# Performance work log

Hardware: AMD Instinct MI355X
Metric: run time of the kernel (lower is better)

Reference implementation:

```python
import jax, jax.numpy as jnp
import numpy as np

D = 1024   # n_embd
H = 16     # n_head
HD = D // H

def setup_inputs() -> dict:
    key = jax.random.key(0)
    ks = jax.random.split(key, 6)
    s = 1.0 / np.sqrt(D)
    x  = jax.random.normal(ks[0], (4, 2048, D), dtype=jnp.float32)
    Wq = jax.random.uniform(ks[1], (D, D), jnp.float32, -s, s)
    Wk = jax.random.uniform(ks[2], (D, D), jnp.float32, -s, s)
    Wv = jax.random.uniform(ks[3], (D, D), jnp.float32, -s, s)
    Wp = jax.random.uniform(ks[4], (D, D), jnp.float32, -s, s)
    bp = jax.random.uniform(ks[5], (D,),   jnp.float32, -s, s)
    return {"x": x, "Wq": Wq, "Wk": Wk, "Wv": Wv, "Wp": Wp, "bp": bp}

def reference(x, Wq, Wk, Wv, Wp, bp):
    B, T, C = x.shape
    scale = 1.0 / np.sqrt(HD)
    # torch nn.Linear: y = x @ W.T
    q = (x @ Wq.T).reshape(B, T, H, HD).transpose(0, 2, 1, 3)  # [B,H,T,hd]
    k = (x @ Wk.T).reshape(B, T, H, HD).transpose(0, 2, 1, 3)
    v = (x @ Wv.T).reshape(B, T, H, HD).transpose(0, 2, 1, 3)
    att = jnp.einsum('bhqd,bhkd->bhqk', q, k) * scale           # [B,H,T,T]
    causal = jnp.tril(jnp.ones((T, T), dtype=bool))
    att = jnp.where(causal[None, None], att, -jnp.inf)
    att = jax.nn.softmax(att, axis=-1)
    y = jnp.einsum('bhqk,bhkd->bhqd', att, v)                   # [B,H,T,hd]
    y = y.transpose(0, 2, 1, 3).reshape(B, T, C)
    return y @ Wp.T + bp
```

## Files before the change

kernel.cpp:

```cpp
#include <hip/hip_runtime.h>
#include <hip/hip_bf16.h>
#include <math.h>


#define B_  4
#define T_  2048
#define D_  1024
#define H_  16
#define HD_ 64
#define M_  (B_ * T_)

typedef short bf16x8 __attribute__((ext_vector_type(8)));
typedef float f32x4  __attribute__((ext_vector_type(4)));

__device__ __forceinline__ f32x4 mfma16(bf16x8 a, bf16x8 b, f32x4 c) {
    return __builtin_amdgcn_mfma_f32_16x16x32_bf16(a, b, c, 0, 0, 0);
}

__device__ __forceinline__ void gl_lds16(const unsigned short* g, unsigned short* l) {
    __builtin_amdgcn_global_load_lds(
        (const __attribute__((address_space(1))) void*)g,
        (__attribute__((address_space(3))) void*)l, 16, 0, 0);
}

__device__ __forceinline__ unsigned short f2bf(float f) {
    union { __hip_bfloat16 h; unsigned short u; } cv;
    cv.h = __float2bfloat16(f);
    return cv.u;
}
__device__ __forceinline__ float bf2f(unsigned short u) {
    return __uint_as_float(((unsigned)u) << 16);
}
__device__ __forceinline__ float exp2_fast(float x) {
    return __builtin_amdgcn_exp2f(x);
}

struct su4 { unsigned short x, y, z, w; };

__global__ __launch_bounds__(256)
void cvt_all_kernel(const float* __restrict__ x,
                    const float* __restrict__ Wq, const float* __restrict__ Wk,
                    const float* __restrict__ Wv, const float* __restrict__ Wp,
                    unsigned short* __restrict__ dst) {
    const int i = blockIdx.x * 256 + threadIdx.x;
    const float* src;
    int j;
    if (i < 2097152) {
        src = x; j = i;
    } else {
        const int k = i - 2097152;
        const int wsel = k >> 18;
        j = k & 262143;
        src = (wsel == 0) ? Wq : (wsel == 1) ? Wk : (wsel == 2) ? Wv : Wp;
    }
    const float4 v = ((const float4*)src)[j];
    su4 o;
    o.x = f2bf(v.x); o.y = f2bf(v.y); o.z = f2bf(v.z); o.w = f2bf(v.w);
    ((su4*)dst)[i] = o;
}

__global__ __launch_bounds__(256, 2)
void qkv_kernel(const unsigned short* __restrict__ X,
                const unsigned short* __restrict__ Wq,
                const unsigned short* __restrict__ Wk,
                const unsigned short* __restrict__ Wv,
                unsigned short* __restrict__ Qo,
                unsigned short* __restrict__ Ko,
                unsigned short* __restrict__ Vo)
{
    __shared__ unsigned short As[128 * 64];
    __shared__ unsigned short Bs[128 * 64];

    const int m0 = blockIdx.x * 128;
    const int by = blockIdx.y;
    const unsigned short* W = (by < 8) ? Wq : (by < 16) ? Wk : Wv;
    unsigned short*       O = (by < 8) ? Qo : (by < 16) ? Ko : Vo;
    const int n0   = (by & 7) * 128;
    const bool vsec = (by >= 16);
    const int tid  = threadIdx.x;
    const int lane = tid & 63;
    const int wv   = tid >> 6;
    const int wr   = (wv >> 1) * 64;
    const int wc   = (wv & 1) * 64;
    const int g    = lane >> 4;
    const int c    = lane & 15;

    f32x4 acc[4][4] = {};

    for (int k0 = 0; k0 < D_; k0 += 64) {
        #pragma unroll
        for (int i = 0; i < 4; ++i) {
            const int flat = i * 2048 + tid * 8;
            const int row = flat >> 6, col = flat & 63;
            gl_lds16(X + (size_t)(m0 + row) * D_ + k0 + col, As + flat);
            gl_lds16(W + (size_t)(n0 + row) * D_ + k0 + col, Bs + flat);
        }
        __syncthreads();
        #pragma unroll
        for (int kk = 0; kk < 64; kk += 32) {
            bf16x8 af[4], bg[4];
            #pragma unroll
            for (int mi = 0; mi < 4; ++mi)
                af[mi] = *(const bf16x8*)(As + (wr + mi * 16 + c) * 64 + kk + g * 8);
            #pragma unroll
            for (int ni = 0; ni < 4; ++ni)
                bg[ni] = *(const bf16x8*)(Bs + (wc + ni * 16 + c) * 64 + kk + g * 8);
            if (!vsec) {
                #pragma unroll
                for (int mi = 0; mi < 4; ++mi)
                    #pragma unroll
                    for (int ni = 0; ni < 4; ++ni)
                        acc[mi][ni] = mfma16(af[mi], bg[ni], acc[mi][ni]);
            } else {
                #pragma unroll
                for (int mi = 0; mi < 4; ++mi)
                    #pragma unroll
                    for (int ni = 0; ni < 4; ++ni)
                        acc[mi][ni] = mfma16(bg[ni], af[mi], acc[mi][ni]);
            }
        }
        __syncthreads();
    }

    if (!vsec) {
        #pragma unroll
        for (int mi = 0; mi < 4; ++mi)
            #pragma unroll
            for (int ni = 0; ni < 4; ++ni)
                #pragma unroll
                for (int r = 0; r < 4; ++r) {
                    const int m = m0 + wr + mi * 16 + g * 4 + r;
                    const int n = n0 + wc + ni * 16 + c;
                    const int b = m >> 11, t = m & (T_ - 1);
                    const int h = n >> 6,  hd = n & 63;
                    O[((size_t)((b << 4) + h) * T_ + t) * HD_ + hd] = f2bf(acc[mi][ni][r]);
                }
    } else {
        #pragma unroll
        for (int mi = 0; mi < 4; ++mi)
            #pragma unroll
            for (int ni = 0; ni < 4; ++ni)
                #pragma unroll
                for (int r = 0; r < 4; ++r) {
                    const int n = n0 + wc + ni * 16 + g * 4 + r;
                    const int m = m0 + wr + mi * 16 + c;
                    const int b = m >> 11, t = m & (T_ - 1);
                    const int h = n >> 6,  hd = n & 63;
                    O[((size_t)((b << 4) + h) * HD_ + hd) * T_ + t] = f2bf(acc[mi][ni][r]);
                }
    }
}

__device__ __forceinline__ bf16x8 ptrans(const f32x4& p0, const f32x4& p1,
                                         int lane, int g, int c) {
    unsigned int P32[2][2];
    P32[0][0] = (unsigned int)f2bf(p0[0]) | ((unsigned int)f2bf(p0[1]) << 16);
    P32[0][1] = (unsigned int)f2bf(p0[2]) | ((unsigned int)f2bf(p0[3]) << 16);
    P32[1][0] = (unsigned int)f2bf(p1[0]) | ((unsigned int)f2bf(p1[1]) << 16);
    P32[1][1] = (unsigned int)f2bf(p1[2]) | ((unsigned int)f2bf(p1[3]) << 16);
    const int sl0 = c + ((lane & 16) << 1);
    const int sl1 = sl0 + 16;
    const int q00 = __shfl((int)P32[0][0], sl0), q10 = __shfl((int)P32[1][0], sl0);
    const int q01 = __shfl((int)P32[0][1], sl0), q11 = __shfl((int)P32[1][1], sl0);
    const int q02 = __shfl((int)P32[0][0], sl1), q12 = __shfl((int)P32[1][0], sl1);
    const int q03 = __shfl((int)P32[0][1], sl1), q13 = __shfl((int)P32[1][1], sl1);
    const bool nhi = (g & 2) != 0;
    union { unsigned int u[4]; bf16x8 v; } pf;
    pf.u[0] = nhi ? q10 : q00;
    pf.u[1] = nhi ? q11 : q01;
    pf.u[2] = nhi ? q12 : q02;
    pf.u[3] = nhi ? q13 : q03;
    return pf.v;
}

__global__ __launch_bounds__(256, 4)
void attn_kernel(const unsigned short* __restrict__ Q,
                 const unsigned short* __restrict__ K,
                 const unsigned short* __restrict__ VT,
                 unsigned short* __restrict__ Y)
{
    __shared__ unsigned short Ks[2][4096];
    __shared__ unsigned short Vs[2][4096];

    const int bh = blockIdx.x;
    const int qt = 31 - blockIdx.y;
    const unsigned short* Qp  = Q  + (size_t)bh * T_ * HD_;
    const unsigned short* Kp  = K  + (size_t)bh * T_ * HD_;
    const unsigned short* VTp = VT + (size_t)bh * HD_ * T_;
    const int b = bh >> 4, h = bh & 15;

    const int tid  = threadIdx.x;
    const int lane = tid & 63;
    const int w    = tid >> 6;
    const int g    = lane >> 4;
    const int c    = lane & 15;
    const float SC = 0.18033688011112042f;

    const int qw = qt * 64 + w * 16;
    const int nt = qt + 1;

    int srow[2], scol[2];
    #pragma unroll
    for (int i = 0; i < 2; ++i) {
        const int L = (i * 256 + tid) * 16;
        srow[i] = L >> 7;
        scol[i] = (L & 127) ^ ((srow[i] & 7) << 4);
    }

    bf16x8 qf[2];
    #pragma unroll
    for (int dk = 0; dk < 2; ++dk) {
        bf16x8 t = *(const bf16x8*)(Qp + (size_t)(qw + c) * HD_ + dk * 32 + g * 8);
        #pragma unroll
        for (int j = 0; j < 8; ++j)
            t[j] = (short)f2bf(bf2f((unsigned short)t[j]) * SC);
        qf[dk] = t;
    }

    float m_l = -1e30f, l_l = 0.f;
    f32x4 oacc[4] = {};
    const int swz = (c & 7) << 4;

    auto stage = [&](int buf, int tb) {
        #pragma unroll
        for (int i = 0; i < 2; ++i) {
            const int L = (i * 256 + tid) * 16;
            gl_lds16(Kp + (size_t)(tb + srow[i]) * HD_ + (scol[i] >> 1),
                     &Ks[buf][L >> 1]);
            gl_lds16(VTp + (size_t)srow[i] * T_ + tb + (scol[i] >> 1),
                     &Vs[buf][L >> 1]);
        }
    };

    auto compute = [&](const unsigned short* Kbuf, const unsigned short* Vbuf,
                       int tb, bool last) {
        const char* Kb = (const char*)Kbuf;
        const char* Vb = (const char*)Vbuf;

        __builtin_amdgcn_s_setprio(1);

        f32x4 sA[2] = {}, sB[2] = {};
        #pragma unroll
        for (int ni = 0; ni < 2; ++ni)
            #pragma unroll
            for (int dk = 0; dk < 2; ++dk) {
                const int col = (dk * 64 + g * 16) ^ swz;
                const bf16x8 kA = *(const bf16x8*)(Kb + (ni * 16 + c) * 128 + col);
                const bf16x8 kB = *(const bf16x8*)(Kb + (32 + ni * 16 + c) * 128 + col);
                sA[ni] = mfma16(kA, qf[dk], sA[ni]);
                sB[ni] = mfma16(kB, qf[dk], sB[ni]);
            }

        if (last) {
            #pragma unroll
            for (int ni = 0; ni < 2; ++ni)
                #pragma unroll
                for (int r = 0; r < 4; ++r) {
                    const int kA = tb + ni * 16 + g * 4 + r;
                    sA[ni][r] = (kA      <= qw + c) ? sA[ni][r] : -1e30f;
                    sB[ni][r] = (kA + 32 <= qw + c) ? sB[ni][r] : -1e30f;
                }
        }

        float pmax = sA[0][0];
        #pragma unroll
        for (int ni = 0; ni < 2; ++ni)
            #pragma unroll
            for (int r = 0; r < 4; ++r) {
                pmax = fmaxf(pmax, sA[ni][r]);
                pmax = fmaxf(pmax, sB[ni][r]);
            }
        pmax = fmaxf(pmax, __shfl_xor(pmax, 16));
        pmax = fmaxf(pmax, __shfl_xor(pmax, 32));

        const bool skip = __all(pmax - m_l <= 8.0f);
        float al = 1.f;
        if (!skip) {
            const float mn = fmaxf(m_l, pmax);
            al = exp2_fast(m_l - mn);
            m_l = mn;
        }

        float rs = 0.f;
        #pragma unroll
        for (int ni = 0; ni < 2; ++ni)
            #pragma unroll
            for (int r = 0; r < 4; ++r) {
                const float eA = exp2_fast(sA[ni][r] - m_l);
                const float eB = exp2_fast(sB[ni][r] - m_l);
                sA[ni][r] = eA; sB[ni][r] = eB;
                rs += eA + eB;
            }
        rs += __shfl_xor(rs, 16);
        rs += __shfl_xor(rs, 32);
        l_l = l_l * al + rs;

        const bf16x8 pfA = ptrans(sA[0], sA[1], lane, g, c);
        const bf16x8 pfB = ptrans(sB[0], sB[1], lane, g, c);

        #pragma unroll
        for (int dn = 0; dn < 4; ++dn) {
            const int row = dn * 16 + c;
            const bf16x8 vA = *(const bf16x8*)(Vb + row * 128 + ((g * 16)      ^ swz));
            const bf16x8 vB = *(const bf16x8*)(Vb + row * 128 + ((64 + g * 16) ^ swz));
            if (!skip) {
                #pragma unroll
                for (int r = 0; r < 4; ++r)
                    oacc[dn][r] *= al;
            }
            oacc[dn] = mfma16(vA, pfA, oacc[dn]);
            oacc[dn] = mfma16(vB, pfB, oacc[dn]);
        }

        __builtin_amdgcn_s_setprio(0);
    };

    stage(0, 0);
    __syncthreads();
    int ti = 0;
    for (;;) {
        if (ti + 1 < nt) stage(1, (ti + 1) << 6);
        compute(Ks[0], Vs[0], ti << 6, ti == nt - 1);
        __syncthreads();
        if (++ti >= nt) break;

        if (ti + 1 < nt) stage(0, (ti + 1) << 6);
        compute(Ks[1], Vs[1], ti << 6, ti == nt - 1);
        __syncthreads();
        if (++ti >= nt) break;
    }

    const float li = 1.f / l_l;
    const size_t rowoff = (size_t)(b * T_ + qw + c) * D_ + h * 64;
    #pragma unroll
    for (int dn = 0; dn < 4; ++dn) {
        const unsigned int u0 = (unsigned int)f2bf(oacc[dn][0] * li)
                              | ((unsigned int)f2bf(oacc[dn][1] * li) << 16);
        const unsigned int u1 = (unsigned int)f2bf(oacc[dn][2] * li)
                              | ((unsigned int)f2bf(oacc[dn][3] * li) << 16);
        uint2 st; st.x = u0; st.y = u1;
        *(uint2*)(Y + rowoff + dn * 16 + g * 4) = st;
    }
}

__global__ __launch_bounds__(256, 2)
void proj_kernel(const unsigned short* __restrict__ Yin,
                 const unsigned short* __restrict__ Wp,
                 const float* __restrict__ bp,
                 float* __restrict__ Out)
{
    __shared__ unsigned short As[128 * 64];
    __shared__ unsigned short Bs[128 * 64];

    const int m0 = blockIdx.x * 128;
    const int n0 = blockIdx.y * 128;
    const int tid  = threadIdx.x;
    const int lane = tid & 63;
    const int wv   = tid >> 6;
    const int wr   = (wv >> 1) * 64;
    const int wc   = (wv & 1) * 64;
    const int g    = lane >> 4;
    const int c    = lane & 15;

    f32x4 acc[4][4] = {};

    for (int k0 = 0; k0 < D_; k0 += 64) {
        #pragma unroll
        for (int i = 0; i < 4; ++i) {
            const int flat = i * 2048 + tid * 8;
            const int row = flat >> 6, col = flat & 63;
            gl_lds16(Yin + (size_t)(m0 + row) * D_ + k0 + col, As + flat);
            gl_lds16(Wp  + (size_t)(n0 + row) * D_ + k0 + col, Bs + flat);
        }
        __syncthreads();
        #pragma unroll
        for (int kk = 0; kk < 64; kk += 32) {
            bf16x8 af[4], bg[4];
            #pragma unroll
            for (int mi = 0; mi < 4; ++mi)
                af[mi] = *(const bf16x8*)(As + (wr + mi * 16 + c) * 64 + kk + g * 8);
            #pragma unroll
            for (int ni = 0; ni < 4; ++ni)
                bg[ni] = *(const bf16x8*)(Bs + (wc + ni * 16 + c) * 64 + kk + g * 8);
            #pragma unroll
            for (int mi = 0; mi < 4; ++mi)
                #pragma unroll
                for (int ni = 0; ni < 4; ++ni)
                    acc[mi][ni] = mfma16(af[mi], bg[ni], acc[mi][ni]);
        }
        __syncthreads();
    }

    #pragma unroll
    for (int mi = 0; mi < 4; ++mi) {
        #pragma unroll
        for (int ni = 0; ni < 4; ++ni) {
            const int n = n0 + wc + ni * 16 + c;
            const float bb = bp[n];
            #pragma unroll
            for (int r = 0; r < 4; ++r) {
                const int m = m0 + wr + mi * 16 + g * 4 + r;
                Out[(size_t)m * D_ + n] = acc[mi][ni][r] + bb;
            }
        }
    }
}

extern "C" void kernel_launch(void* const* d_in, const int* in_sizes, int n_in,
                              void* d_out, int out_size, void* d_ws, size_t ws_size,
                              hipStream_t stream) {
    const float* x  = (const float*)d_in[0];
    const float* Wq = (const float*)d_in[1];
    const float* Wk = (const float*)d_in[2];
    const float* Wv = (const float*)d_in[3];
    const float* Wp = (const float*)d_in[4];
    const float* bp = (const float*)d_in[5];
    float* out = (float*)d_out;

    const size_t SZ  = (size_t)M_ * D_;
    const size_t WSZ = (size_t)D_ * D_;
    unsigned short* ws = (unsigned short*)d_ws;
    unsigned short* XB  = ws;
    unsigned short* WQB = XB  + SZ;
    unsigned short* WKB = WQB + WSZ;
    unsigned short* WVB = WKB + WSZ;
    unsigned short* WPB = WVB + WSZ;
    unsigned short* Qw  = WPB + WSZ;
    unsigned short* Kw  = Qw + SZ;
    unsigned short* Vw  = Kw + SZ;
    unsigned short* Yw  = XB;

    dim3 blk(256);
    cvt_all_kernel<<<dim3(12288), blk, 0, stream>>>(x, Wq, Wk, Wv, Wp, ws);

    qkv_kernel <<<dim3(M_ / 128, 24), blk, 0, stream>>>(XB, WQB, WKB, WVB, Qw, Kw, Vw);
    attn_kernel<<<dim3(B_ * H_, T_ / 64), blk, 0, stream>>>(Qw, Kw, Vw, Yw);
    proj_kernel<<<dim3(M_ / 128, D_ / 128), blk, 0, stream>>>(Yw, WPB, bp, out);
}
```

Before: 194.5 us.

## Switch attention to 32x32x16 MFMA with 128-row query tiles per block

Rewrites the attention kernel so each wave handles 32 query rows using the 32x32x16 bf16 MFMA, and each block covers 128 queries instead of 64. Each K/V tile staged in LDS now serves twice as many queries, and the P transpose needs only a single xor-32 shuffle instead of the multi-shuffle ptrans routine. Waves whose rows lie entirely before a key tile skip its compute, and causal masking is applied only on diagonal tiles. The grid halves to 1024 blocks, which reduces parallelism and adds more causal imbalance within a block, and the larger accumulators raise register pressure.

```diff
diff --git a/kernel.cpp b/kernel.cpp
--- a/kernel.cpp
+++ b/kernel.cpp
@@ -12,9 +12,13 @@
 
 typedef short bf16x8 __attribute__((ext_vector_type(8)));
 typedef float f32x4  __attribute__((ext_vector_type(4)));
+typedef float f32x16 __attribute__((ext_vector_type(16)));
 
 __device__ __forceinline__ f32x4 mfma16(bf16x8 a, bf16x8 b, f32x4 c) {
     return __builtin_amdgcn_mfma_f32_16x16x32_bf16(a, b, c, 0, 0, 0);
+}
+__device__ __forceinline__ f32x16 mfma32(bf16x8 a, bf16x8 b, f32x16 c) {
+    return __builtin_amdgcn_mfma_f32_32x32x16_bf16(a, b, c, 0, 0, 0);
 }
 
 __device__ __forceinline__ void gl_lds16(const unsigned short* g, unsigned short* l) {
@@ -151,28 +155,6 @@
     }
 }
 
-__device__ __forceinline__ bf16x8 ptrans(const f32x4& p0, const f32x4& p1,
-                                         int lane, int g, int c) {
-    unsigned int P32[2][2];
-    P32[0][0] = (unsigned int)f2bf(p0[0]) | ((unsigned int)f2bf(p0[1]) << 16);
-    P32[0][1] = (unsigned int)f2bf(p0[2]) | ((unsigned int)f2bf(p0[3]) << 16);
-    P32[1][0] = (unsigned int)f2bf(p1[0]) | ((unsigned int)f2bf(p1[1]) << 16);
-    P32[1][1] = (unsigned int)f2bf(p1[2]) | ((unsigned int)f2bf(p1[3]) << 16);
-    const int sl0 = c + ((lane & 16) << 1);
-    const int sl1 = sl0 + 16;
-    const int q00 = __shfl((int)P32[0][0], sl0), q10 = __shfl((int)P32[1][0], sl0);
-    const int q01 = __shfl((int)P32[0][1], sl0), q11 = __shfl((int)P32[1][1], sl0);
-    const int q02 = __shfl((int)P32[0][0], sl1), q12 = __shfl((int)P32[1][0], sl1);
-    const int q03 = __shfl((int)P32[0][1], sl1), q13 = __shfl((int)P32[1][1], sl1);
-    const bool nhi = (g & 2) != 0;
-    union { unsigned int u[4]; bf16x8 v; } pf;
-    pf.u[0] = nhi ? q10 : q00;
-    pf.u[1] = nhi ? q11 : q01;
-    pf.u[2] = nhi ? q12 : q02;
-    pf.u[3] = nhi ? q13 : q03;
-    return pf.v;
-}
-
 __global__ __launch_bounds__(256, 4)
 void attn_kernel(const unsigned short* __restrict__ Q,
                  const unsigned short* __restrict__ K,
@@ -183,7 +165,7 @@
     __shared__ unsigned short Vs[2][4096];
 
     const int bh = blockIdx.x;
-    const int qt = 31 - blockIdx.y;
+    const int qt = 15 - blockIdx.y;
     const unsigned short* Qp  = Q  + (size_t)bh * T_ * HD_;
     const unsigned short* Kp  = K  + (size_t)bh * T_ * HD_;
     const unsigned short* VTp = VT + (size_t)bh * HD_ * T_;
@@ -192,12 +174,12 @@
     const int tid  = threadIdx.x;
     const int lane = tid & 63;
     const int w    = tid >> 6;
-    const int g    = lane >> 4;
-    const int c    = lane & 15;
+    const int hi   = lane >> 5;
+    const int q31  = lane & 31;
     const float SC = 0.18033688011112042f;
 
-    const int qw = qt * 64 + w * 16;
-    const int nt = qt + 1;
+    const int qw = qt * 128 + w * 32;
+    const int nt = 2 * qt + 2;
 
     int srow[2], scol[2];
     #pragma unroll
@@ -207,19 +189,19 @@
         scol[i] = (L & 127) ^ ((srow[i] & 7) << 4);
     }
 
-    bf16x8 qf[2];
+    bf16x8 qf[4];
     #pragma unroll
-    for (int dk = 0; dk < 2; ++dk) {
-        bf16x8 t = *(const bf16x8*)(Qp + (size_t)(qw + c) * HD_ + dk * 32 + g * 8);
+    for (int dstep = 0; dstep < 4; ++dstep) {
+        bf16x8 t = *(const bf16x8*)(Qp + (size_t)(qw + q31) * HD_ + dstep * 16 + hi * 8);
         #pragma unroll
         for (int j = 0; j < 8; ++j)
             t[j] = (short)f2bf(bf2f((unsigned short)t[j]) * SC);
-        qf[dk] = t;
+        qf[dstep] = t;
     }
 
     float m_l = -1e30f, l_l = 0.f;
-    f32x4 oacc[4] = {};
-    const int swz = (c & 7) << 4;
+    f32x16 o0 = {}, o1 = {};
+    const int swz = (lane & 7) << 4;
 
     auto stage = [&](int buf, int tb) {
         #pragma unroll
@@ -232,45 +214,38 @@
         }
     };
 
-    auto compute = [&](const unsigned short* Kbuf, const unsigned short* Vbuf,
-                       int tb, bool last) {
+    auto compute = [&](const unsigned short* Kbuf, const unsigned short* Vbuf, int tb) {
+        if (tb > qw + 31) return;
         const char* Kb = (const char*)Kbuf;
         const char* Vb = (const char*)Vbuf;
 
         __builtin_amdgcn_s_setprio(1);
 
-        f32x4 sA[2] = {}, sB[2] = {};
-        #pragma unroll
-        for (int ni = 0; ni < 2; ++ni)
-            #pragma unroll
-            for (int dk = 0; dk < 2; ++dk) {
-                const int col = (dk * 64 + g * 16) ^ swz;
-                const bf16x8 kA = *(const bf16x8*)(Kb + (ni * 16 + c) * 128 + col);
-                const bf16x8 kB = *(const bf16x8*)(Kb + (32 + ni * 16 + c) * 128 + col);
-                sA[ni] = mfma16(kA, qf[dk], sA[ni]);
-                sB[ni] = mfma16(kB, qf[dk], sB[ni]);
+        f32x16 s0 = {}, s1 = {};
+        #pragma unroll
+        for (int dstep = 0; dstep < 4; ++dstep) {
+            const int col = (dstep * 32 + hi * 16) ^ swz;
+            const bf16x8 kA = *(const bf16x8*)(Kb + q31 * 128 + col);
+            const bf16x8 kB = *(const bf16x8*)(Kb + (32 + q31) * 128 + col);
+            s0 = mfma32(kA, qf[dstep], s0);
+            s1 = mfma32(kB, qf[dstep], s1);
+        }
+
+        if (tb + 63 > qw) {
+            const int qq = qw + q31;
+            #pragma unroll
+            for (int r = 0; r < 16; ++r) {
+                const int key = tb + (r & 3) + 8 * (r >> 2) + 4 * hi;
+                s0[r] = (key      <= qq) ? s0[r] : -1e30f;
+                s1[r] = (key + 32 <= qq) ? s1[r] : -1e30f;
             }
-
-        if (last) {
-            #pragma unroll
-            for (int ni = 0; ni < 2; ++ni)
-                #pragma unroll
-                for (int r = 0; r < 4; ++r) {
-                    const int kA = tb + ni * 16 + g * 4 + r;
-                    sA[ni][r] = (kA      <= qw + c) ? sA[ni][r] : -1e30f;
-                    sB[ni][r] = (kA + 32 <= qw + c) ? sB[ni][r] : -1e30f;
-                }
-        }
-
-        float pmax = sA[0][0];
-        #pragma unroll
-        for (int ni = 0; ni < 2; ++ni)
-            #pragma unroll
-            for (int r = 0; r < 4; ++r) {
-                pmax = fmaxf(pmax, sA[ni][r]);
-                pmax = fmaxf(pmax, sB[ni][r]);
-            }
-        pmax = fmaxf(pmax, __shfl_xor(pmax, 16));
+        }
+
+        float pmax = s0[0];
+        #pragma unroll
+        for (int r = 1; r < 16; ++r) pmax = fmaxf(pmax, s0[r]);
+        #pragma unroll
+        for (int r = 0; r < 16; ++r) pmax = fmaxf(pmax, s1[r]);
         pmax = fmaxf(pmax, __shfl_xor(pmax, 32));
 
         const bool skip = __all(pmax - m_l <= 8.0f);
@@ -283,33 +258,64 @@
 
         float rs = 0.f;
         #pragma unroll
-        for (int ni = 0; ni < 2; ++ni)
-            #pragma unroll
-            for (int r = 0; r < 4; ++r) {
-                const float eA = exp2_fast(sA[ni][r] - m_l);
-                const float eB = exp2_fast(sB[ni][r] - m_l);
-                sA[ni][r] = eA; sB[ni][r] = eB;
-                rs += eA + eB;
-            }
-        rs += __shfl_xor(rs, 16);
+        for (int r = 0; r < 16; ++r) {
+            const float e0 = exp2_fast(s0[r] - m_l);
+            const float e1 = exp2_fast(s1[r] - m_l);
+            s0[r] = e0; s1[r] = e1;
+            rs += e0 + e1;
+        }
         rs += __shfl_xor(rs, 32);
         l_l = l_l * al + rs;
 
-        const bf16x8 pfA = ptrans(sA[0], sA[1], lane, g, c);
-        const bf16x8 pfB = ptrans(sB[0], sB[1], lane, g, c);
-
-        #pragma unroll
-        for (int dn = 0; dn < 4; ++dn) {
-            const int row = dn * 16 + c;
-            const bf16x8 vA = *(const bf16x8*)(Vb + row * 128 + ((g * 16)      ^ swz));
-            const bf16x8 vB = *(const bf16x8*)(Vb + row * 128 + ((64 + g * 16) ^ swz));
-            if (!skip) {
-                #pragma unroll
-                for (int r = 0; r < 4; ++r)
-                    oacc[dn][r] *= al;
-            }
-            oacc[dn] = mfma16(vA, pfA, oacc[dn]);
-            oacc[dn] = mfma16(vB, pfB, oacc[dn]);
+        unsigned Glo0[4], Ghi0[4], Glo1[4], Ghi1[4];
+        #pragma unroll
+        for (int m = 0; m < 4; ++m) {
+            Glo0[m] = (unsigned)f2bf(s0[4*m])   | ((unsigned)f2bf(s0[4*m+1]) << 16);
+            Ghi0[m] = (unsigned)f2bf(s0[4*m+2]) | ((unsigned)f2bf(s0[4*m+3]) << 16);
+            Glo1[m] = (unsigned)f2bf(s1[4*m])   | ((unsigned)f2bf(s1[4*m+1]) << 16);
+            Ghi1[m] = (unsigned)f2bf(s1[4*m+2]) | ((unsigned)f2bf(s1[4*m+3]) << 16);
+        }
+        unsigned PGlo0[4], PGhi0[4], PGlo1[4], PGhi1[4];
+        #pragma unroll
+        for (int m = 0; m < 4; ++m) {
+            PGlo0[m] = (unsigned)__shfl_xor((int)Glo0[m], 32);
+            PGhi0[m] = (unsigned)__shfl_xor((int)Ghi0[m], 32);
+            PGlo1[m] = (unsigned)__shfl_xor((int)Glo1[m], 32);
+            PGhi1[m] = (unsigned)__shfl_xor((int)Ghi1[m], 32);
+        }
+
+        bf16x8 pf[4];
+        #pragma unroll
+        for (int ks = 0; ks < 4; ++ks) {
+            const int m0i = 2 * (ks & 1);
+            const int m1i = m0i + 1;
+            const unsigned gl0 = (ks < 2) ? Glo0[m0i] : Glo1[m0i];
+            const unsigned gh0 = (ks < 2) ? Ghi0[m0i] : Ghi1[m0i];
+            const unsigned gl1 = (ks < 2) ? Glo0[m1i] : Glo1[m1i];
+            const unsigned gh1 = (ks < 2) ? Ghi0[m1i] : Ghi1[m1i];
+            const unsigned pl0 = (ks < 2) ? PGlo0[m0i] : PGlo1[m0i];
+            const unsigned ph0 = (ks < 2) ? PGhi0[m0i] : PGhi1[m0i];
+            const unsigned pl1 = (ks < 2) ? PGlo0[m1i] : PGlo1[m1i];
+            const unsigned ph1 = (ks < 2) ? PGhi0[m1i] : PGhi1[m1i];
+            union { unsigned u[4]; bf16x8 v; } pp;
+            pp.u[0] = hi ? pl1 : gl0;
+            pp.u[1] = hi ? ph1 : gh0;
+            pp.u[2] = hi ? gl1 : pl0;
+            pp.u[3] = hi ? gh1 : ph0;
+            pf[ks] = pp.v;
+        }
+
+        if (!skip) {
+            #pragma unroll
+            for (int r = 0; r < 16; ++r) { o0[r] *= al; o1[r] *= al; }
+        }
+        #pragma unroll
+        for (int ks = 0; ks < 4; ++ks) {
+            const int col = (ks * 32 + hi * 16) ^ swz;
+            const bf16x8 vA = *(const bf16x8*)(Vb + q31 * 128 + col);
+            const bf16x8 vB = *(const bf16x8*)(Vb + (32 + q31) * 128 + col);
+            o0 = mfma32(vA, pf[ks], o0);
+            o1 = mfma32(vB, pf[ks], o1);
         }
 
         __builtin_amdgcn_s_setprio(0);
@@ -317,29 +323,26 @@
 
     stage(0, 0);
     __syncthreads();
-    int ti = 0;
-    for (;;) {
-        if (ti + 1 < nt) stage(1, (ti + 1) << 6);
-        compute(Ks[0], Vs[0], ti << 6, ti == nt - 1);
-        __syncthreads();
-        if (++ti >= nt) break;
-
-        if (ti + 1 < nt) stage(0, (ti + 1) << 6);
-        compute(Ks[1], Vs[1], ti << 6, ti == nt - 1);
-        __syncthreads();
-        if (++ti >= nt) break;
+    for (int ti = 0; ti < nt; ti += 2) {
+        stage(1, (ti + 1) << 6);
+        compute(Ks[0], Vs[0], ti << 6);
+        __syncthreads();
+        if (ti + 2 < nt) stage(0, (ti + 2) << 6);
+        compute(Ks[1], Vs[1], (ti + 1) << 6);
+        __syncthreads();
     }
 
     const float li = 1.f / l_l;
-    const size_t rowoff = (size_t)(b * T_ + qw + c) * D_ + h * 64;
+    const size_t rowoff = (size_t)(b * T_ + qw + q31) * D_ + h * 64;
     #pragma unroll
-    for (int dn = 0; dn < 4; ++dn) {
-        const unsigned int u0 = (unsigned int)f2bf(oacc[dn][0] * li)
-                              | ((unsigned int)f2bf(oacc[dn][1] * li) << 16);
-        const unsigned int u1 = (unsigned int)f2bf(oacc[dn][2] * li)
-                              | ((unsigned int)f2bf(oacc[dn][3] * li) << 16);
-        uint2 st; st.x = u0; st.y = u1;
-        *(uint2*)(Y + rowoff + dn * 16 + g * 4) = st;
+    for (int t = 0; t < 4; ++t) {
+        uint2 st0, st1;
+        st0.x = (unsigned)f2bf(o0[4*t]   * li) | ((unsigned)f2bf(o0[4*t+1] * li) << 16);
+        st0.y = (unsigned)f2bf(o0[4*t+2] * li) | ((unsigned)f2bf(o0[4*t+3] * li) << 16);
+        st1.x = (unsigned)f2bf(o1[4*t]   * li) | ((unsigned)f2bf(o1[4*t+1] * li) << 16);
+        st1.y = (unsigned)f2bf(o1[4*t+2] * li) | ((unsigned)f2bf(o1[4*t+3] * li) << 16);
+        *(uint2*)(Y + rowoff      + 8 * t + 4 * hi) = st0;
+        *(uint2*)(Y + rowoff + 32 + 8 * t + 4 * hi) = st1;
     }
 }
 
@@ -434,6 +437,6 @@
     cvt_all_kernel<<<dim3(12288), blk, 0, stream>>>(x, Wq, Wk, Wv, Wp, ws);
 
     qkv_kernel <<<dim3(M_ / 128, 24), blk, 0, stream>>>(XB, WQB, WKB, WVB, Qw, Kw, Vw);
-    attn_kernel<<<dim3(B_ * H_, T_ / 64), blk, 0, stream>>>(Qw, Kw, Vw, Yw);
+    attn_kernel<<<dim3(B_ * H_, 16), blk, 0, stream>>>(Qw, Kw, Vw, Yw);
     proj_kernel<<<dim3(M_ / 128, D_ / 128), blk, 0, stream>>>(Yw, WPB, bp, out);
 }
```

Result: faster. 180.5 us (median of 3 runs) (-7.2%).
